# Kernel optimization log

Measured on AMD Instinct MI355X. Metric: run time of the kernel, lower is better.

## Reference

```python
import jax, jax.numpy as jnp
import numpy as np

B, N, M, D = 64, 16384, 64, 512
EPS = 1e-16


def setup_inputs() -> dict:
    key = jax.random.key(0)
    k1, k2, k3, k4 = jax.random.split(key, 4)
    controller_output = jax.random.normal(k1, (B, D), dtype=jnp.float32)
    w_prev = jax.random.uniform(k2, (B, N), dtype=jnp.float32)
    memory = jax.random.normal(k3, (B, N, M), dtype=jnp.float32)
    W = jax.random.normal(k4, (M + 6, D), dtype=jnp.float32) * (1.0 / np.sqrt(D))
    b = jnp.zeros((M + 6,), dtype=jnp.float32)
    return {"controller_output": controller_output, "w_prev": w_prev,
            "memory": memory, "W": W, "b": b}


def reference(controller_output, w_prev, memory, W, b):
    # fc_read projection -> [B, M+6], split into k, beta, g, s, gamma
    o = controller_output @ W.T + b
    k = o[:, :M]                      # [B, M] content key
    beta = jax.nn.softplus(o[:, M:M + 1])        # [B, 1] key strength
    g = jax.nn.sigmoid(o[:, M + 1:M + 2])        # [B, 1] interpolation gate
    s = jax.nn.softmax(o[:, M + 2:M + 5], axis=1)  # [B, 3] shift weights
    gamma = 1.0 + jax.nn.softplus(o[:, M + 5:M + 6])  # [B, 1] sharpening

    # content addressing: cosine similarity between k and each memory row
    num = jnp.einsum('bm,bnm->bn', k, memory)                      # [B, N]
    denom = (jnp.linalg.norm(k, axis=1, keepdims=True)
             * jnp.linalg.norm(memory, axis=2) + EPS)              # [B, N]
    w_c = jax.nn.softmax(beta * (num / denom), axis=1)             # [B, N]

    # interpolation with previous weighting
    w_g = g * w_c + (1.0 - g) * w_prev                              # [B, N]

    # circular convolution shift over {-1, 0, +1}
    w_t = (s[:, 0:1] * jnp.roll(w_g, 1, axis=1)
           + s[:, 1:2] * w_g
           + s[:, 2:3] * jnp.roll(w_g, -1, axis=1))                 # [B, N]

    # sharpening
    w_pow = w_t ** gamma
    w = w_pow / (jnp.sum(w_pow, axis=1, keepdims=True) + EPS)       # [B, N]

    # read: weighted sum of memory rows
    r = jnp.einsum('bn,bnm->bm', w, memory)                         # [B, M]
    return (r, w)
```

## Files before the change

kernel.cpp:

```cpp
#include <hip/hip_runtime.h>
#include <math.h>

#define B 64
#define N 16384
#define MDIM 64
#define DDIM 512
#define EPSF 1e-16f
#define NCH 32
#define CHUNK 512
#define GRID (B * NCH)

#define K_OFF      0
#define SCAL_OFF   (B*64)
#define SCORE_OFF  (SCAL_OFF + B*8)
#define MS_OFF     (SCORE_OFF + B*N)
#define PSUM_OFF   (MS_OFF + B*NCH*2)
#define PART_OFF   (PSUM_OFF + B*NCH)

__device__ __forceinline__ float rowsum16(float x) {
    float t;
    t = __int_as_float(__builtin_amdgcn_update_dpp(0, __float_as_int(x), 0x128, 0xF, 0xF, true)); x += t;
    t = __int_as_float(__builtin_amdgcn_update_dpp(0, __float_as_int(x), 0x124, 0xF, 0xF, true)); x += t;
    t = __int_as_float(__builtin_amdgcn_update_dpp(0, __float_as_int(x), 0x122, 0xF, 0xF, true)); x += t;
    t = __int_as_float(__builtin_amdgcn_update_dpp(0, __float_as_int(x), 0x121, 0xF, 0xF, true)); x += t;
    return x;
}

__global__ __launch_bounds__(256) void k1(const float* __restrict__ c,
                                          const float* __restrict__ W,
                                          const float* __restrict__ bias,
                                          float* __restrict__ ws) {
    int b = blockIdx.x;
    __shared__ float cs[DDIM];
    __shared__ float osh[72];
    int tid = threadIdx.x;
    for (int i = tid; i < DDIM; i += 256) cs[i] = c[b * DDIM + i];
    __syncthreads();
    int wave = tid >> 6, lane = tid & 63;
    for (int j = wave; j < MDIM + 6; j += 4) {
        const float* wr = W + (size_t)j * DDIM;
        float sum = 0.f;
        for (int d = lane; d < DDIM; d += 64) sum += cs[d] * wr[d];
        for (int off = 32; off > 0; off >>= 1) sum += __shfl_xor(sum, off);
        if (lane == 0) osh[j] = sum + bias[j];
    }
    __syncthreads();
    if (tid < 64) ws[K_OFF + b * 64 + tid] = osh[tid];
    if (wave == 0) {
        float v = osh[lane];
        float sq = v * v;
        for (int off = 32; off > 0; off >>= 1) sq += __shfl_xor(sq, off);
        if (lane == 0) {
            float kn = sqrtf(sq);
            float ob = osh[64], og = osh[65], os0 = osh[66], os1 = osh[67],
                  os2 = osh[68], ogm = osh[69];
            float beta  = fmaxf(ob, 0.f) + log1pf(expf(-fabsf(ob)));
            float g     = 1.f / (1.f + expf(-og));
            float mx    = fmaxf(os0, fmaxf(os1, os2));
            float e0 = expf(os0 - mx), e1 = expf(os1 - mx), e2 = expf(os2 - mx);
            float es = e0 + e1 + e2;
            float gamma = 1.f + fmaxf(ogm, 0.f) + log1pf(expf(-fabsf(ogm)));
            float* sc = ws + SCAL_OFF + b * 8;
            sc[0] = kn; sc[1] = beta; sc[2] = g;
            sc[3] = e0 / es; sc[4] = e1 / es; sc[5] = e2 / es;
            sc[6] = gamma;
        }
    }
}

__global__ __launch_bounds__(256) void k2(const float* __restrict__ mem,
                                          float* __restrict__ ws) {
    int b = blockIdx.x >> 5, chunk = blockIdx.x & 31;
    __shared__ float ks[64];
    __shared__ float kb2[2];
    __shared__ float scbuf[CHUNK];
    int tid = threadIdx.x;
    if (tid < 64) ks[tid] = ws[K_OFF + b * 64 + tid];
    if (tid == 64) kb2[0] = ws[SCAL_OFF + b * 8 + 0];
    if (tid == 65) kb2[1] = ws[SCAL_OFF + b * 8 + 1];
    __syncthreads();
    float kn = kb2[0], beta = kb2[1];
    int grp = tid >> 4, ll = tid & 15;
    float k0 = ks[ll * 4], k1v = ks[ll * 4 + 1], k2v = ks[ll * 4 + 2], k3v = ks[ll * 4 + 3];
    int row0 = chunk * CHUNK;
    #pragma unroll 8
    for (int it = 0; it < CHUNK / 16; ++it) {
        int lrow = it * 16 + grp;
        float4 v = *reinterpret_cast<const float4*>(
            mem + ((size_t)b * N + row0 + lrow) * MDIM + ll * 4);
        float dot = v.x * k0 + v.y * k1v + v.z * k2v + v.w * k3v;
        float sq  = v.x * v.x + v.y * v.y + v.z * v.z + v.w * v.w;
        dot = rowsum16(dot);
        sq  = rowsum16(sq);
        if (ll == 0)
            scbuf[lrow] = beta * (dot / (kn * sqrtf(sq) + EPSF));
    }
    __syncthreads();
    {
        float s0v = scbuf[tid], s1v = scbuf[tid + 256];
        float* sco = ws + SCORE_OFF + (size_t)b * N + row0;
        sco[tid] = s0v;
        sco[tid + 256] = s1v;
    }
    if (tid < 64) {
        float vr[8];
        float m = -1e30f;
        #pragma unroll
        for (int j = 0; j < 8; ++j) {
            vr[j] = scbuf[tid + 64 * j];
            m = fmaxf(m, vr[j]);
        }
        #pragma unroll
        for (int off = 32; off > 0; off >>= 1) m = fmaxf(m, __shfl_xor(m, off));
        float s = 0.f;
        #pragma unroll
        for (int j = 0; j < 8; ++j) s += __expf(vr[j] - m);
        #pragma unroll
        for (int off = 32; off > 0; off >>= 1) s += __shfl_xor(s, off);
        if (tid == 0) {
            ws[MS_OFF + ((size_t)b * NCH + chunk) * 2]     = m;
            ws[MS_OFF + ((size_t)b * NCH + chunk) * 2 + 1] = s;
        }
    }
}

__global__ __launch_bounds__(256) void krw(const float* __restrict__ mem,
                                           const float* __restrict__ w_prev,
                                           float* __restrict__ ws,
                                           float* __restrict__ w_out,
                                           float* __restrict__ part) {
    int b = blockIdx.x >> 5, chunk = blockIdx.x & 31;
    int tid = threadIdx.x, wave = tid >> 6, lane = tid & 63;
    __shared__ float wgL[CHUNK + 2];
    __shared__ float wpl[CHUNK];
    __shared__ float lds[16][64];
    __shared__ float red[4];
    const float* sl = ws + SCAL_OFF + b * 8;
    float g = sl[2], s0 = sl[3], s1 = sl[4], s2 = sl[5], gamma = sl[6];

    float mx = -1e30f, ssum = 0.f;
    const float* msp = ws + MS_OFF + (size_t)b * NCH * 2;
    #pragma unroll
    for (int i = 0; i < NCH; ++i) {
        float mi = msp[i * 2], si = msp[i * 2 + 1];
        float M = fmaxf(mx, mi);
        ssum = ssum * __expf(mx - M) + si * __expf(mi - M);
        mx = M;
    }
    float inv = 1.f / ssum;

    const float* sc = ws + SCORE_OFF + (size_t)b * N;
    const float* wp = w_prev + (size_t)b * N;
    int row0 = chunk * CHUNK;

    {
        int r0 = row0 + tid;
        wgL[tid + 1]   = g * (__expf(sc[r0] - mx) * inv) + (1.f - g) * wp[r0];
        int r1 = row0 + tid + 256;
        wgL[tid + 257] = g * (__expf(sc[r1] - mx) * inv) + (1.f - g) * wp[r1];
        if (tid == 0) {
            int rl = (row0 - 1) & (N - 1);
            wgL[0] = g * (__expf(sc[rl] - mx) * inv) + (1.f - g) * wp[rl];
        }
        if (tid == 255) {
            int rr = (row0 + CHUNK) & (N - 1);
            wgL[CHUNK + 1] = g * (__expf(sc[rr] - mx) * inv) + (1.f - g) * wp[rr];
        }
    }
    __syncthreads();

    float wt0 = s0 * wgL[tid]       + s1 * wgL[tid + 1]   + s2 * wgL[tid + 2];
    float wt1 = s0 * wgL[tid + 256] + s1 * wgL[tid + 257] + s2 * wgL[tid + 258];
    float p0 = __expf(gamma * __logf(wt0));
    float p1 = __expf(gamma * __logf(wt1));
    wpl[tid] = p0;
    wpl[tid + 256] = p1;
    float* wo = w_out + (size_t)b * N + row0;
    wo[tid]       = p0;
    wo[tid + 256] = p1;

    float sp = p0 + p1;
    #pragma unroll
    for (int off = 32; off > 0; off >>= 1) sp += __shfl_xor(sp, off);
    if (lane == 0) red[wave] = sp;
    __syncthreads();
    if (tid == 0)
        ws[PSUM_OFF + (size_t)b * NCH + chunk] = red[0] + red[1] + red[2] + red[3];

    int grp = tid >> 4, ll = tid & 15;
    float4 acc = make_float4(0.f, 0.f, 0.f, 0.f);
    #pragma unroll 8
    for (int it = 0; it < CHUNK / 16; ++it) {
        int lrow = it * 16 + grp;
        float wv = wpl[lrow];
        float4 v = *reinterpret_cast<const float4*>(
            mem + ((size_t)b * N + row0 + lrow) * MDIM + ll * 4);
        acc.x += wv * v.x; acc.y += wv * v.y; acc.z += wv * v.z; acc.w += wv * v.w;
    }
    lds[grp][ll * 4 + 0] = acc.x;
    lds[grp][ll * 4 + 1] = acc.y;
    lds[grp][ll * 4 + 2] = acc.z;
    lds[grp][ll * 4 + 3] = acc.w;
    __syncthreads();
    if (tid < 64) {
        float sacc = 0.f;
        #pragma unroll
        for (int gi = 0; gi < 16; ++gi) sacc += lds[gi][tid];
        part[(size_t)blockIdx.x * 64 + tid] = sacc;
    }
}

__global__ __launch_bounds__(256) void kfin(const float* __restrict__ part,
                                            float* __restrict__ ws,
                                            float* __restrict__ w_out,
                                            float* __restrict__ r) {
    int b = blockIdx.x >> 5, chunk = blockIdx.x & 31;
    int tid = threadIdx.x;
    __shared__ float invps;
    if (tid < 64) {
        float s = (tid < 32) ? ws[PSUM_OFF + (size_t)b * NCH + tid] : 0.f;
        #pragma unroll
        for (int off = 32; off > 0; off >>= 1) s += __shfl_xor(s, off);
        if (tid == 0) invps = 1.f / (s + EPSF);
    }
    __syncthreads();
    float invp = invps;
    size_t base = (size_t)b * N + chunk * CHUNK;
    w_out[base + tid]       *= invp;
    w_out[base + tid + 256] *= invp;
    if (chunk == 0 && tid < 64) {
        float srr = 0.f;
        #pragma unroll
        for (int c2 = 0; c2 < NCH; ++c2)
            srr += part[((size_t)b * NCH + c2) * 64 + tid];
        r[b * 64 + tid] = srr * invp;
    }
}

extern "C" void kernel_launch(void* const* d_in, const int* in_sizes, int n_in,
                              void* d_out, int out_size, void* d_ws, size_t ws_size,
                              hipStream_t stream) {
    const float* c      = (const float*)d_in[0];
    const float* w_prev = (const float*)d_in[1];
    const float* mem    = (const float*)d_in[2];
    const float* W      = (const float*)d_in[3];
    const float* bias   = (const float*)d_in[4];
    float* out = (float*)d_out;
    float* r_out = out;
    float* w_out = out + B * MDIM;
    float* ws = (float*)d_ws;
    float* part = ws + PART_OFF;

    k1  <<<B,    256, 0, stream>>>(c, W, bias, ws);
    k2  <<<GRID, 256, 0, stream>>>(mem, ws);
    krw <<<GRID, 256, 0, stream>>>(mem, w_prev, ws, w_out, part);
    kfin<<<GRID, 256, 0, stream>>>(part, ws, w_out, r_out);
}
```

Measured before the change: 111.0 us.

## Prefetch memory rows in read kernel before softmax prologue, use nontemporal loads

The read kernel now issues the first four float4 loads of its memory chunk before it computes the softmax normalisation and the shift and sharpening prologue, then keeps a four-deep register ring of in-flight loads through the weighted-sum loop. The intent is to hide global-memory latency behind the prologue. The serial 32-step merge of per-chunk max/sum is replaced by a wave-level butterfly shuffle reduction. Launch bounds request 8 blocks per CU for both k2 and krw, and the loads are marked nontemporal. The added live registers could hurt occupancy or force spills under the tighter launch bound.

```diff
diff --git a/kernel.cpp b/kernel.cpp
--- a/kernel.cpp
+++ b/kernel.cpp
@@ -9,6 +9,8 @@
 #define NCH 32
 #define CHUNK 512
 #define GRID (B * NCH)
+
+typedef float f4 __attribute__((ext_vector_type(4)));
 
 #define K_OFF      0
 #define SCAL_OFF   (B*64)
@@ -68,8 +70,8 @@
     }
 }
 
-__global__ __launch_bounds__(256) void k2(const float* __restrict__ mem,
-                                          float* __restrict__ ws) {
+__global__ __launch_bounds__(256, 8) void k2(const float* __restrict__ mem,
+                                             float* __restrict__ ws) {
     int b = blockIdx.x >> 5, chunk = blockIdx.x & 31;
     __shared__ float ks[64];
     __shared__ float kb2[2];
@@ -124,34 +126,47 @@
     }
 }
 
-__global__ __launch_bounds__(256) void krw(const float* __restrict__ mem,
-                                           const float* __restrict__ w_prev,
-                                           float* __restrict__ ws,
-                                           float* __restrict__ w_out,
-                                           float* __restrict__ part) {
+__global__ __launch_bounds__(256, 8) void krw(const float* __restrict__ mem,
+                                              const float* __restrict__ w_prev,
+                                              float* __restrict__ ws,
+                                              float* __restrict__ w_out,
+                                              float* __restrict__ part) {
     int b = blockIdx.x >> 5, chunk = blockIdx.x & 31;
     int tid = threadIdx.x, wave = tid >> 6, lane = tid & 63;
+    int grp = tid >> 4, ll = tid & 15;
     __shared__ float wgL[CHUNK + 2];
     __shared__ float wpl[CHUNK];
     __shared__ float lds[16][64];
     __shared__ float red[4];
+    int row0 = chunk * CHUNK;
+
+    const f4* mbase = (const f4*)(mem + ((size_t)b * N + row0 + grp) * MDIM + ll * 4);
+    f4 pre[4];
+    #pragma unroll
+    for (int j = 0; j < 4; ++j)
+        pre[j] = __builtin_nontemporal_load(mbase + j * 256);
+
     const float* sl = ws + SCAL_OFF + b * 8;
     float g = sl[2], s0 = sl[3], s1 = sl[4], s2 = sl[5], gamma = sl[6];
 
-    float mx = -1e30f, ssum = 0.f;
     const float* msp = ws + MS_OFF + (size_t)b * NCH * 2;
-    #pragma unroll
-    for (int i = 0; i < NCH; ++i) {
-        float mi = msp[i * 2], si = msp[i * 2 + 1];
-        float M = fmaxf(mx, mi);
-        ssum = ssum * __expf(mx - M) + si * __expf(mi - M);
-        mx = M;
-    }
-    float inv = 1.f / ssum;
+    float mi = -1e30f, si = 0.f;
+    if (lane < NCH) {
+        mi = msp[lane * 2];
+        si = msp[lane * 2 + 1];
+    }
+    #pragma unroll
+    for (int off = 32; off > 0; off >>= 1) {
+        float m2 = __shfl_xor(mi, off), s2x = __shfl_xor(si, off);
+        float M = fmaxf(mi, m2);
+        si = si * __expf(mi - M) + s2x * __expf(m2 - M);
+        mi = M;
+    }
+    float mx = mi;
+    float inv = 1.f / si;
 
     const float* sc = ws + SCORE_OFF + (size_t)b * N;
     const float* wp = w_prev + (size_t)b * N;
-    int row0 = chunk * CHUNK;
 
     {
         int r0 = row0 + tid;
@@ -187,15 +202,15 @@
     if (tid == 0)
         ws[PSUM_OFF + (size_t)b * NCH + chunk] = red[0] + red[1] + red[2] + red[3];
 
-    int grp = tid >> 4, ll = tid & 15;
-    float4 acc = make_float4(0.f, 0.f, 0.f, 0.f);
-    #pragma unroll 8
+    f4 acc = (f4)(0.f);
+    #pragma unroll
     for (int it = 0; it < CHUNK / 16; ++it) {
-        int lrow = it * 16 + grp;
-        float wv = wpl[lrow];
-        float4 v = *reinterpret_cast<const float4*>(
-            mem + ((size_t)b * N + row0 + lrow) * MDIM + ll * 4);
-        acc.x += wv * v.x; acc.y += wv * v.y; acc.z += wv * v.z; acc.w += wv * v.w;
+        f4 v = pre[it & 3];
+        int nxt = it + 4;
+        if (nxt < CHUNK / 16)
+            pre[it & 3] = __builtin_nontemporal_load(mbase + nxt * 256);
+        float wv = wpl[it * 16 + grp];
+        acc += wv * v;
     }
     lds[grp][ll * 4 + 0] = acc.x;
     lds[grp][ll * 4 + 1] = acc.y;
```

After: 109.0 us. No clear change (-1.8%).
